# Kernel optimization log

Measured on AMD Instinct MI355X. Metric: run time of the kernel, lower is better.

## Reference

```python
import jax, jax.numpy as jnp
import numpy as np

B, T, D, R = 4, 2048, 512, 1024
N_INNER, N_B = 9, 2          # inner pool bins, boundary pool bins (roipool_size='2_9')
RATIO = 1.0 / 5.0            # boundary extension ratio passed to BRoI1DPool
NB = N_B + N_INNER + N_B     # 13 total bins: [start bins | inner bins | end bins]


def _bin_centers(a, b, n):
    # a, b: (B, R) -> (B, R, n) centers of n equal bins covering [a, b]
    i = (jnp.arange(n, dtype=a.dtype) + 0.5) / n
    return a[..., None] + i * (b - a)[..., None]


def broi1d_pool(feats, rois):
    # Boundary ROI 1D pooling: feats (B, T, D), rois (B, R, 2) -> (B, R, D, NB).
    # Each bin samples its center position via linear interpolation along T.
    s, e = rois[..., 0], rois[..., 1]
    ext = RATIO * (e - s)
    pos = jnp.concatenate([
        _bin_centers(s - ext, s + ext, N_B),
        _bin_centers(s, e, N_INNER),
        _bin_centers(e - ext, e + ext, N_B)], axis=-1)          # (B, R, NB)
    pos = jnp.clip(pos, 0.0, T - 1)
    lo = jnp.floor(pos).astype(jnp.int32)
    hi = jnp.minimum(lo + 1, T - 1)
    w = (pos - lo.astype(pos.dtype))[..., None]

    def gather(idx):
        g = jnp.take_along_axis(feats, idx.reshape(idx.shape[0], -1)[..., None], axis=1)
        return g.reshape(idx.shape + (feats.shape[-1],))          # (B, R, NB, D)

    vals = (1.0 - w) * gather(lo) + w * gather(hi)
    return vals.transpose(0, 1, 3, 2)                              # (B, R, D, NB)


def setup_inputs():
    key = jax.random.key(0)
    ks = jax.random.split(key, 10)
    features = jax.random.normal(ks[0], (B, T, D), jnp.float32)

    def make_rois(k):
        k1, k2 = jax.random.split(k)
        s = jax.random.uniform(k1, (B, R), jnp.float32, 0.0, T - 300.0)
        L = 16.0 + jax.random.uniform(k2, (B, R), jnp.float32) * 256.0
        return jnp.stack([s, s + L], axis=-1)

    rois = make_rois(ks[1])
    start_rois = make_rois(ks[2])
    end_rois = make_rois(ks[3])
    rois_mask = jnp.ones((B, R), jnp.float32)
    rois_pos_emb = jax.random.normal(ks[4], (B, R, D), jnp.float32)

    d_left = (N_B + N_INNER // 2 + 1) * D
    W_left = jax.random.normal(ks[5], (D, d_left), jnp.float32) / np.sqrt(d_left).astype(np.float32)
    b_left = jnp.zeros((D,), jnp.float32)
    W_inner = jax.random.normal(ks[6], (D, N_INNER * D), jnp.float32) / np.sqrt(N_INNER * D).astype(np.float32)
    b_inner = jnp.zeros((D,), jnp.float32)
    W_roi = jax.random.normal(ks[7], (D, 2 * D), jnp.float32) / np.sqrt(2 * D).astype(np.float32)
    b_roi = jnp.zeros((D,), jnp.float32)
    return {"features": features, "start_rois": start_rois, "end_rois": end_rois,
            "rois": rois, "rois_mask": rois_mask, "rois_pos_emb": rois_pos_emb,
            "W_left": W_left, "b_left": b_left, "W_inner": W_inner, "b_inner": b_inner,
            "W_roi": W_roi, "b_roi": b_roi}


def reference(features, start_rois, end_rois, rois, rois_mask, rois_pos_emb,
              W_left, b_left, W_inner, b_inner, W_roi, b_roi):
    pooled = broi1d_pool(features, rois)          # (B, R, D, NB)
    mb, r = pooled.shape[:2]

    def fc(x, W, b):
        # Linear + Dropout(eval=identity) + SELU
        return jax.nn.selu(x @ W.T + b)

    left = fc(pooled[:, :, :, 0:N_INNER // 2 + N_B + 1].reshape(mb, r, -1), W_left, b_left)
    inner = fc(pooled[:, :, :, N_B:N_INNER + N_B].reshape(mb, r, -1), W_inner, b_inner)
    # NOTE: the original code reuses left_fc for the right branch (right_fc is dead).
    right = fc(pooled[:, :, :, N_INNER // 2 + N_B:N_INNER + 2 * N_B].reshape(mb, r, -1), W_left, b_left)
    return fc(jnp.concatenate([right - left, inner], axis=2), W_roi, b_roi)  # (B, R, D)
```

## Files before the change

kernel.cpp:

```cpp
#include <hip/hip_runtime.h>
#include <hip/hip_bf16.h>
#include <cstdint>
#include <cmath>

#define BB 4
#define TT 2048
#define DD 512
#define RR 1024
#define MM (BB*RR)
#define NBINS 13
#define LDXP (NBINS*DD)

typedef __bf16 bf16;
typedef bf16 bf16x8 __attribute__((ext_vector_type(8)));
typedef bf16 bf16x2 __attribute__((ext_vector_type(2)));
typedef float f32x4 __attribute__((ext_vector_type(4)));

__device__ __forceinline__ float selu_f(float x) {
    const float sc = 1.0507009873554805f;
    const float aa = 1.6732632423543772f;
    return x > 0.0f ? sc * x : sc * aa * (expf(x) - 1.0f);
}

__device__ __forceinline__ void gload_lds16(const bf16* g, bf16* l) {
    __builtin_amdgcn_global_load_lds(
        (const __attribute__((address_space(1))) void*)g,
        (__attribute__((address_space(3))) void*)l, 16, 0, 0);
}

template<int N>
__device__ __forceinline__ void wait_vm() {
    if constexpr (N == 0)      asm volatile("s_waitcnt vmcnt(0)" ::: "memory");
    else if constexpr (N == 4) asm volatile("s_waitcnt vmcnt(4)" ::: "memory");
    else if constexpr (N == 6) asm volatile("s_waitcnt vmcnt(6)" ::: "memory");
}

template<int ROWS>
__device__ __forceinline__ void stage_tile64(const bf16* __restrict__ src, int lda,
                                             bf16* tile, int tid) {
#pragma unroll
    for (int it = 0; it < ROWS / 32; ++it) {
        int idx = it * 256 + tid;
        int row = idx >> 3;
        int col = ((idx & 7) ^ (row & 7)) * 8;
        bf16* wavebase = tile + (idx & ~63) * 8;
        gload_lds16(src + (size_t)row * lda + col, wavebase);
    }
}

__device__ __forceinline__ bf16x8 frd64(const bf16* tile, int row, int s) {
    int p = s ^ (row & 7);
    return *(const bf16x8*)(tile + row * 64 + p * 8);
}

template<int NB_, int KT>
__device__ __forceinline__ void w_row_body(const float* __restrict__ Wsrc,
                                           bf16* __restrict__ Wdst,
                                           float* ld, int n, int tid) {
    const float* src = Wsrc + (size_t)n * KT;
    for (int i = tid; i < KT; i += 256) ld[i] = src[i];
    __syncthreads();
    bf16* dst = Wdst + (size_t)n * KT;
    for (int i = tid; i < KT; i += 256) {
        int bin = i >> 9, d = i & 511;
        dst[i] = (bf16)ld[d * NB_ + bin];
    }
}

__device__ __forceinline__ void pool_body(const float* __restrict__ feats,
                                          const float* __restrict__ rois,
                                          bf16* __restrict__ Xp, int m, int tid) {
    int b = m >> 10;
    float s = rois[2 * m];
    float e = rois[2 * m + 1];
    float ext = 0.2f * (e - s);
    int d0 = tid * 2;
    bf16* orow = Xp + (size_t)m * LDXP + d0;
    const float* fb = feats + (size_t)b * TT * DD + d0;
#pragma unroll
    for (int j = 0; j < NBINS; ++j) {
        float pos;
        if (j < 2)       pos = (s - ext) + ((float)j + 0.5f) * ext;
        else if (j < 11) pos = s + (((float)(j - 2) + 0.5f) * (1.0f / 9.0f)) * (e - s);
        else             pos = (e - ext) + ((float)(j - 11) + 0.5f) * ext;
        pos = fminf(fmaxf(pos, 0.0f), (float)(TT - 1));
        float fl = floorf(pos);
        int lo = (int)fl;
        int hi = lo + 1; if (hi > TT - 1) hi = TT - 1;
        float w = pos - fl;
        float2 vlo = *(const float2*)(fb + (size_t)lo * DD);
        float2 vhi = *(const float2*)(fb + (size_t)hi * DD);
        bf16x2 o;
        o.x = (bf16)((1.0f - w) * vlo.x + w * vhi.x);
        o.y = (bf16)((1.0f - w) * vlo.y + w * vhi.y);
        *(bf16x2*)(orow + j * DD) = o;
    }
}

__global__ __launch_bounds__(256) void prep_all(
    const float* __restrict__ feats, const float* __restrict__ rois,
    const float* __restrict__ W_left, const float* __restrict__ W_inner,
    const float* __restrict__ W_roi,
    bf16* __restrict__ Xp, bf16* __restrict__ Wl, bf16* __restrict__ Wi,
    bf16* __restrict__ Wr)
{
    __shared__ float ld[4608];
    int bid = blockIdx.x, tid = threadIdx.x;
    if (bid < 4096) {
        pool_body(feats, rois, Xp, bid, tid);
    } else if (bid < 4608) {
        w_row_body<7, 3584>(W_left, Wl, ld, bid - 4096, tid);
    } else if (bid < 5120) {
        w_row_body<9, 4608>(W_inner, Wi, ld, bid - 4608, tid);
    } else {
        int i0 = (bid - 5120) * 1024 + tid * 4;
        float4 v = *(const float4*)(W_roi + i0);
        bf16* d = Wr + i0;
        d[0] = (bf16)v.x; d[1] = (bf16)v.y; d[2] = (bf16)v.z; d[3] = (bf16)v.w;
    }
}


template<int K, bool OUT_BF16>
__device__ __forceinline__ void gemm_single_body(
    const bf16* __restrict__ A, int lda,
    const bf16* __restrict__ Bw, const float* __restrict__ bias,
    void* __restrict__ Out, int ldo, int ocol0,
    bf16* sm, int m0, int n0)
{
    int tid = threadIdx.x, lane = tid & 63, w = tid >> 6;
    int wr = w >> 1, wc = w & 1;
    const bf16* Ab = A + (size_t)m0 * lda;
    const bf16* Bb = Bw + (size_t)n0 * K;
    int frow = lane & 15, sl = lane >> 4;
    f32x4 acc[2][2] = {};
    bf16 *A0 = sm,        *B0 = sm + 4096;
    bf16 *A1 = sm + 8192, *B1 = sm + 12288;

    auto stage = [&](bf16* ap, bf16* bp, int t) {
        stage_tile64<64>(Ab + t * 64, lda, ap, tid);
        stage_tile64<64>(Bb + t * 64, K, bp, tid);
    };
    auto step = [&](bf16* ap, bf16* bp, int t, bool dostage) {
        __builtin_amdgcn_s_barrier();
        bf16x8 af[2][2], bfr[2][2];
#pragma unroll
        for (int ks = 0; ks < 2; ++ks) {
#pragma unroll
            for (int mf = 0; mf < 2; ++mf) af[ks][mf] = frd64(ap, wr * 32 + mf * 16 + frow, ks * 4 + sl);
#pragma unroll
            for (int nf = 0; nf < 2; ++nf) bfr[ks][nf] = frd64(bp, wc * 32 + nf * 16 + frow, ks * 4 + sl);
        }
        asm volatile("s_waitcnt lgkmcnt(0)" ::: "memory");
        __builtin_amdgcn_sched_barrier(0);
        __builtin_amdgcn_s_barrier();
        if (dostage) stage(ap, bp, t + 2);
        __builtin_amdgcn_s_setprio(1);
#pragma unroll
        for (int ks = 0; ks < 2; ++ks)
#pragma unroll
            for (int mf = 0; mf < 2; ++mf)
#pragma unroll
                for (int nf = 0; nf < 2; ++nf)
                    acc[mf][nf] = __builtin_amdgcn_mfma_f32_16x16x32_bf16(af[ks][mf], bfr[ks][nf], acc[mf][nf], 0, 0, 0);
        __builtin_amdgcn_s_setprio(0);
    };

    constexpr int NT = K / 64;
    stage(A0, B0, 0);
    stage(A1, B1, 1);
    for (int t = 0; t + 2 < NT; t += 2) {
        wait_vm<4>(); step(A0, B0, t, true);
        wait_vm<4>(); step(A1, B1, t + 1, true);
    }
    wait_vm<4>(); step(A0, B0, NT - 2, false);
    wait_vm<0>(); step(A1, B1, NT - 1, false);

    int crow = (lane >> 4) * 4;
    int ccol = lane & 15;
#pragma unroll
    for (int mf = 0; mf < 2; ++mf) {
#pragma unroll
        for (int nf = 0; nf < 2; ++nf) {
            int col = n0 + wc * 32 + nf * 16 + ccol;
            float bv = bias[col];
#pragma unroll
            for (int r2 = 0; r2 < 4; ++r2) {
                int row = m0 + wr * 32 + mf * 16 + crow + r2;
                float v = selu_f(acc[mf][nf][r2] + bv);
                if constexpr (OUT_BF16)
                    ((bf16*)Out)[(size_t)row * ldo + ocol0 + col] = (bf16)v;
                else
                    ((float*)Out)[(size_t)row * ldo + ocol0 + col] = v;
            }
        }
    }
}

template<int K>
__device__ __forceinline__ void gemm_dual_body(
    const bf16* __restrict__ Xp, const bf16* __restrict__ Wl,
    const float* __restrict__ bias, bf16* __restrict__ Y,
    bf16* sm, int m0, int n0)
{
    int tid = threadIdx.x, lane = tid & 63, w = tid >> 6;
    int wr = w >> 1, wc = w & 1;
    const bf16* AL = Xp + (size_t)m0 * LDXP;
    const bf16* AR = AL + 3072;
    const bf16* Bb = Wl + (size_t)n0 * K;
    int frow = lane & 15, sl = lane >> 4;
    f32x4 accL[2][2] = {}, accR[2][2] = {};
    bf16 *L0 = sm,         *R0 = sm + 4096,  *B0 = sm + 8192;
    bf16 *L1 = sm + 12288, *R1 = sm + 16384, *B1 = sm + 20480;

    auto stage = [&](bf16* lp, bf16* rp, bf16* bp, int t) {
        stage_tile64<64>(AL + t * 64, LDXP, lp, tid);
        stage_tile64<64>(AR + t * 64, LDXP, rp, tid);
        stage_tile64<64>(Bb + t * 64, K, bp, tid);
    };
    auto step = [&](bf16* lp, bf16* rp, bf16* bp, int t, bool dostage) {
        __builtin_amdgcn_s_barrier();
        bf16x8 afL[2][2], afR[2][2], bfr[2][2];
#pragma unroll
        for (int ks = 0; ks < 2; ++ks) {
#pragma unroll
            for (int mf = 0; mf < 2; ++mf) {
                afL[ks][mf] = frd64(lp, wr * 32 + mf * 16 + frow, ks * 4 + sl);
                afR[ks][mf] = frd64(rp, wr * 32 + mf * 16 + frow, ks * 4 + sl);
            }
#pragma unroll
            for (int nf = 0; nf < 2; ++nf) bfr[ks][nf] = frd64(bp, wc * 32 + nf * 16 + frow, ks * 4 + sl);
        }
        asm volatile("s_waitcnt lgkmcnt(0)" ::: "memory");
        __builtin_amdgcn_sched_barrier(0);
        __builtin_amdgcn_s_barrier();
        if (dostage) stage(lp, rp, bp, t + 2);
        __builtin_amdgcn_s_setprio(1);
#pragma unroll
        for (int ks = 0; ks < 2; ++ks)
#pragma unroll
            for (int mf = 0; mf < 2; ++mf)
#pragma unroll
                for (int nf = 0; nf < 2; ++nf) {
                    accL[mf][nf] = __builtin_amdgcn_mfma_f32_16x16x32_bf16(afL[ks][mf], bfr[ks][nf], accL[mf][nf], 0, 0, 0);
                    accR[mf][nf] = __builtin_amdgcn_mfma_f32_16x16x32_bf16(afR[ks][mf], bfr[ks][nf], accR[mf][nf], 0, 0, 0);
                }
        __builtin_amdgcn_s_setprio(0);
    };

    constexpr int NT = K / 64;
    stage(L0, R0, B0, 0);
    stage(L1, R1, B1, 1);
    for (int t = 0; t + 2 < NT; t += 2) {
        wait_vm<6>(); step(L0, R0, B0, t, true);
        wait_vm<6>(); step(L1, R1, B1, t + 1, true);
    }
    wait_vm<6>(); step(L0, R0, B0, NT - 2, false);
    wait_vm<0>(); step(L1, R1, B1, NT - 1, false);

    int crow = (lane >> 4) * 4;
    int ccol = lane & 15;
#pragma unroll
    for (int mf = 0; mf < 2; ++mf) {
#pragma unroll
        for (int nf = 0; nf < 2; ++nf) {
            int col = n0 + wc * 32 + nf * 16 + ccol;
            float bv = bias[col];
#pragma unroll
            for (int r2 = 0; r2 < 4; ++r2) {
                int row = m0 + wr * 32 + mf * 16 + crow + r2;
                float vL = selu_f(accL[mf][nf][r2] + bv);
                float vR = selu_f(accR[mf][nf][r2] + bv);
                Y[(size_t)row * 1024 + col] = (bf16)(vR - vL);
            }
        }
    }
}

__global__ __launch_bounds__(256) void wide_gemm(
    const bf16* __restrict__ Xp, const bf16* __restrict__ Wl,
    const float* __restrict__ bl, const bf16* __restrict__ Wi,
    const float* __restrict__ bi, bf16* __restrict__ Y)
{
    __shared__ bf16 sm[24576];
    int bid = blockIdx.x;
    if (bid < 512) {
        gemm_dual_body<3584>(Xp, Wl, bl, Y, sm, (bid & 63) * 64, (bid >> 6) * 64);
    } else {
        int b2 = bid - 512;
        gemm_single_body<4608, true>(Xp + 1024, LDXP, Wi, bi, (void*)Y, 1024, 512,
                                     sm, (b2 & 63) * 64, (b2 >> 6) * 64);
    }
}

__global__ __launch_bounds__(256) void final_gemm(
    const bf16* __restrict__ Y, const bf16* __restrict__ Wr,
    const float* __restrict__ br, float* __restrict__ out)
{
    __shared__ bf16 sm[16384];
    int bid = blockIdx.x;
    gemm_single_body<1024, false>(Y, 1024, Wr, br, (void*)out, 512, 0,
                                  sm, (bid & 63) * 64, (bid >> 6) * 64);
}

extern "C" void kernel_launch(void* const* d_in, const int* in_sizes, int n_in,
                              void* d_out, int out_size, void* d_ws, size_t ws_size,
                              hipStream_t stream) {
    const float* feats   = (const float*)d_in[0];
    const float* rois    = (const float*)d_in[3];
    const float* W_left  = (const float*)d_in[6];
    const float* b_left  = (const float*)d_in[7];
    const float* W_inner = (const float*)d_in[8];
    const float* b_inner = (const float*)d_in[9];
    const float* W_roi   = (const float*)d_in[10];
    const float* b_roi   = (const float*)d_in[11];
    float* out = (float*)d_out;

    bf16* wsb = (bf16*)d_ws;
    constexpr size_t XP_ELEMS = (size_t)MM * LDXP;
    constexpr size_t WL_ELEMS = (size_t)512 * 3584;
    constexpr size_t WI_ELEMS = (size_t)512 * 4608;
    constexpr size_t WR_ELEMS = (size_t)512 * 1024;
    bf16* Xp = wsb;
    bf16* Wl = Xp + XP_ELEMS;
    bf16* Wi = Wl + WL_ELEMS;
    bf16* Wr = Wi + WI_ELEMS;
    bf16* Y  = Wr + WR_ELEMS;

    prep_all<<<5632, 256, 0, stream>>>(feats, rois, W_left, W_inner, W_roi,
                                       Xp, Wl, Wi, Wr);
    wide_gemm<<<1024, 256, 0, stream>>>(Xp, Wl, b_left, Wi, b_inner, Y);
    final_gemm<<<512, 256, 0, stream>>>(Y, Wr, b_roi, out);
}
```

Before: 113.3 us.

## Enlarge GEMM tiles to 128x64 and pipeline K in 32-wide half-tile stages

The GEMM tiles grow from 64x64 to 128x64 rows per block, and each 64-wide K step is split into two 32-wide halves with their own swizzle. Loads of the next half are interleaved with MFMA work on the current half under finer vmcnt waits and barriers. This is meant to raise operand reuse per LDS load and hide global latency better. In exchange it halves the grid (512 and 256 blocks on a 256-CU part), raises LDS and accumulator register use, and adds more barriers per K step.

```diff
diff --git a/kernel.cpp b/kernel.cpp
--- a/kernel.cpp
+++ b/kernel.cpp
@@ -30,27 +30,34 @@
 
 template<int N>
 __device__ __forceinline__ void wait_vm() {
-    if constexpr (N == 0)      asm volatile("s_waitcnt vmcnt(0)" ::: "memory");
-    else if constexpr (N == 4) asm volatile("s_waitcnt vmcnt(4)" ::: "memory");
-    else if constexpr (N == 6) asm volatile("s_waitcnt vmcnt(6)" ::: "memory");
+    if constexpr (N == 0)       asm volatile("s_waitcnt vmcnt(0)" ::: "memory");
+    else if constexpr (N == 3)  asm volatile("s_waitcnt vmcnt(3)" ::: "memory");
+    else if constexpr (N == 5)  asm volatile("s_waitcnt vmcnt(5)" ::: "memory");
+    else if constexpr (N == 6)  asm volatile("s_waitcnt vmcnt(6)" ::: "memory");
+    else if constexpr (N == 10) asm volatile("s_waitcnt vmcnt(10)" ::: "memory");
+}
+
+__device__ __forceinline__ void lgkm_fence() {
+    asm volatile("s_waitcnt lgkmcnt(0)" ::: "memory");
+    __builtin_amdgcn_sched_barrier(0);
 }
 
 template<int ROWS>
-__device__ __forceinline__ void stage_tile64(const bf16* __restrict__ src, int lda,
-                                             bf16* tile, int tid) {
-#pragma unroll
-    for (int it = 0; it < ROWS / 32; ++it) {
+__device__ __forceinline__ void stage_half(const bf16* __restrict__ src, int lda,
+                                           bf16* dst, int tid) {
+#pragma unroll
+    for (int it = 0; it < ROWS / 64; ++it) {
         int idx = it * 256 + tid;
-        int row = idx >> 3;
-        int col = ((idx & 7) ^ (row & 7)) * 8;
-        bf16* wavebase = tile + (idx & ~63) * 8;
+        int row = idx >> 2;
+        int col = ((idx & 3) ^ ((row >> 1) & 3)) * 8;
+        bf16* wavebase = dst + (idx & ~63) * 8;
         gload_lds16(src + (size_t)row * lda + col, wavebase);
     }
 }
 
-__device__ __forceinline__ bf16x8 frd64(const bf16* tile, int row, int s) {
-    int p = s ^ (row & 7);
-    return *(const bf16x8*)(tile + row * 64 + p * 8);
+__device__ __forceinline__ bf16x8 frd32(const bf16* half, int row, int sl) {
+    int p = sl ^ ((row >> 1) & 3);
+    return *(const bf16x8*)(half + row * 32 + p * 8);
 }
 
 template<int NB_, int KT>
@@ -133,60 +140,74 @@
     const bf16* Ab = A + (size_t)m0 * lda;
     const bf16* Bb = Bw + (size_t)n0 * K;
     int frow = lane & 15, sl = lane >> 4;
-    f32x4 acc[2][2] = {};
-    bf16 *A0 = sm,        *B0 = sm + 4096;
-    bf16 *A1 = sm + 8192, *B1 = sm + 12288;
-
-    auto stage = [&](bf16* ap, bf16* bp, int t) {
-        stage_tile64<64>(Ab + t * 64, lda, ap, tid);
-        stage_tile64<64>(Bb + t * 64, K, bp, tid);
-    };
-    auto step = [&](bf16* ap, bf16* bp, int t, bool dostage) {
-        __builtin_amdgcn_s_barrier();
-        bf16x8 af[2][2], bfr[2][2];
-#pragma unroll
-        for (int ks = 0; ks < 2; ++ks) {
-#pragma unroll
-            for (int mf = 0; mf < 2; ++mf) af[ks][mf] = frd64(ap, wr * 32 + mf * 16 + frow, ks * 4 + sl);
-#pragma unroll
-            for (int nf = 0; nf < 2; ++nf) bfr[ks][nf] = frd64(bp, wc * 32 + nf * 16 + frow, ks * 4 + sl);
-        }
-        asm volatile("s_waitcnt lgkmcnt(0)" ::: "memory");
-        __builtin_amdgcn_sched_barrier(0);
-        __builtin_amdgcn_s_barrier();
-        if (dostage) stage(ap, bp, t + 2);
+    f32x4 acc[4][2] = {};
+    bf16 *buf0 = sm, *buf1 = sm + 12288;
+
+    auto stageH = [&](bf16* p, int u, int h) {
+        stage_half<128>(Ab + u * 64 + h * 32, lda, p + h * 4096, tid);
+        stage_half<64>(Bb + u * 64 + h * 32, K, p + 8192 + h * 2048, tid);
+    };
+    auto rdA = [&](bf16* p, int h, bf16x8 (&af)[4]) {
+#pragma unroll
+        for (int mf = 0; mf < 4; ++mf)
+            af[mf] = frd32(p + h * 4096, wr * 64 + mf * 16 + frow, sl);
+    };
+    auto rdB = [&](bf16* p, int h, bf16x8 (&bfr)[2]) {
+#pragma unroll
+        for (int nf = 0; nf < 2; ++nf)
+            bfr[nf] = frd32(p + 8192 + h * 2048, wc * 32 + nf * 16 + frow, sl);
+    };
+    auto mm = [&](bf16x8 (&af)[4], bf16x8 (&bfr)[2]) {
         __builtin_amdgcn_s_setprio(1);
 #pragma unroll
-        for (int ks = 0; ks < 2; ++ks)
-#pragma unroll
-            for (int mf = 0; mf < 2; ++mf)
-#pragma unroll
-                for (int nf = 0; nf < 2; ++nf)
-                    acc[mf][nf] = __builtin_amdgcn_mfma_f32_16x16x32_bf16(af[ks][mf], bfr[ks][nf], acc[mf][nf], 0, 0, 0);
+        for (int mf = 0; mf < 4; ++mf)
+#pragma unroll
+            for (int nf = 0; nf < 2; ++nf)
+                acc[mf][nf] = __builtin_amdgcn_mfma_f32_16x16x32_bf16(af[mf], bfr[nf], acc[mf][nf], 0, 0, 0);
         __builtin_amdgcn_s_setprio(0);
     };
 
+    auto tileS = [&](bf16* b, bf16* nb, int t, int mode) {
+        bf16x8 af[4], bfr[2];
+        if (mode <= 1) stageH(nb, t + 1, 1);
+        rdA(b, 0, af); rdB(b, 0, bfr);
+        if (mode <= 1) wait_vm<6>(); else wait_vm<0>();
+        __builtin_amdgcn_s_barrier();
+        lgkm_fence();
+        mm(af, bfr);
+        __builtin_amdgcn_s_barrier();
+        if (mode == 0) stageH(b, t + 2, 0);
+        rdA(b, 1, af); rdB(b, 1, bfr);
+        if (mode == 0) wait_vm<6>(); else if (mode == 1) wait_vm<3>();
+        __builtin_amdgcn_s_barrier();
+        lgkm_fence();
+        mm(af, bfr);
+        __builtin_amdgcn_s_barrier();
+    };
+
     constexpr int NT = K / 64;
-    stage(A0, B0, 0);
-    stage(A1, B1, 1);
-    for (int t = 0; t + 2 < NT; t += 2) {
-        wait_vm<4>(); step(A0, B0, t, true);
-        wait_vm<4>(); step(A1, B1, t + 1, true);
-    }
-    wait_vm<4>(); step(A0, B0, NT - 2, false);
-    wait_vm<0>(); step(A1, B1, NT - 1, false);
+    stageH(buf0, 0, 0); stageH(buf0, 0, 1); stageH(buf1, 1, 0);
+    wait_vm<6>();
+    __builtin_amdgcn_s_barrier();
+    int t = 0;
+    for (; t + 2 < NT; ++t) {
+        bf16 *b = (t & 1) ? buf1 : buf0, *nb = (t & 1) ? buf0 : buf1;
+        tileS(b, nb, t, 0);
+    }
+    { bf16 *b = (t & 1) ? buf1 : buf0, *nb = (t & 1) ? buf0 : buf1; tileS(b, nb, t, 1); ++t; }
+    { bf16 *b = (t & 1) ? buf1 : buf0, *nb = (t & 1) ? buf0 : buf1; tileS(b, nb, t, 2); }
 
     int crow = (lane >> 4) * 4;
     int ccol = lane & 15;
 #pragma unroll
-    for (int mf = 0; mf < 2; ++mf) {
+    for (int mf = 0; mf < 4; ++mf) {
 #pragma unroll
         for (int nf = 0; nf < 2; ++nf) {
             int col = n0 + wc * 32 + nf * 16 + ccol;
             float bv = bias[col];
 #pragma unroll
             for (int r2 = 0; r2 < 4; ++r2) {
-                int row = m0 + wr * 32 + mf * 16 + crow + r2;
+                int row = m0 + wr * 64 + mf * 16 + crow + r2;
                 float v = selu_f(acc[mf][nf][r2] + bv);
                 if constexpr (OUT_BF16)
                     ((bf16*)Out)[(size_t)row * ldo + ocol0 + col] = (bf16)v;
@@ -209,66 +230,90 @@
     const bf16* AR = AL + 3072;
     const bf16* Bb = Wl + (size_t)n0 * K;
     int frow = lane & 15, sl = lane >> 4;
-    f32x4 accL[2][2] = {}, accR[2][2] = {};
-    bf16 *L0 = sm,         *R0 = sm + 4096,  *B0 = sm + 8192;
-    bf16 *L1 = sm + 12288, *R1 = sm + 16384, *B1 = sm + 20480;
-
-    auto stage = [&](bf16* lp, bf16* rp, bf16* bp, int t) {
-        stage_tile64<64>(AL + t * 64, LDXP, lp, tid);
-        stage_tile64<64>(AR + t * 64, LDXP, rp, tid);
-        stage_tile64<64>(Bb + t * 64, K, bp, tid);
-    };
-    auto step = [&](bf16* lp, bf16* rp, bf16* bp, int t, bool dostage) {
-        __builtin_amdgcn_s_barrier();
-        bf16x8 afL[2][2], afR[2][2], bfr[2][2];
-#pragma unroll
-        for (int ks = 0; ks < 2; ++ks) {
-#pragma unroll
-            for (int mf = 0; mf < 2; ++mf) {
-                afL[ks][mf] = frd64(lp, wr * 32 + mf * 16 + frow, ks * 4 + sl);
-                afR[ks][mf] = frd64(rp, wr * 32 + mf * 16 + frow, ks * 4 + sl);
-            }
-#pragma unroll
-            for (int nf = 0; nf < 2; ++nf) bfr[ks][nf] = frd64(bp, wc * 32 + nf * 16 + frow, ks * 4 + sl);
-        }
-        asm volatile("s_waitcnt lgkmcnt(0)" ::: "memory");
-        __builtin_amdgcn_sched_barrier(0);
-        __builtin_amdgcn_s_barrier();
-        if (dostage) stage(lp, rp, bp, t + 2);
+    f32x4 accL[4][2] = {}, accR[4][2] = {};
+    bf16 *buf0 = sm, *buf1 = sm + 20480;
+
+    auto stageH = [&](bf16* p, int u, int h) {
+        stage_half<128>(AL + u * 64 + h * 32, LDXP, p + h * 4096, tid);
+        stage_half<128>(AR + u * 64 + h * 32, LDXP, p + 8192 + h * 4096, tid);
+        stage_half<64>(Bb + u * 64 + h * 32, K, p + 16384 + h * 2048, tid);
+    };
+    auto rdL = [&](bf16* p, int h, bf16x8 (&af)[4]) {
+#pragma unroll
+        for (int mf = 0; mf < 4; ++mf)
+            af[mf] = frd32(p + h * 4096, wr * 64 + mf * 16 + frow, sl);
+    };
+    auto rdR = [&](bf16* p, int h, bf16x8 (&af)[4]) {
+#pragma unroll
+        for (int mf = 0; mf < 4; ++mf)
+            af[mf] = frd32(p + 8192 + h * 4096, wr * 64 + mf * 16 + frow, sl);
+    };
+    auto rdB = [&](bf16* p, int h, bf16x8 (&bfr)[2]) {
+#pragma unroll
+        for (int nf = 0; nf < 2; ++nf)
+            bfr[nf] = frd32(p + 16384 + h * 2048, wc * 32 + nf * 16 + frow, sl);
+    };
+    auto mm = [&](bf16x8 (&af)[4], bf16x8 (&bfr)[2], f32x4 (&ac)[4][2]) {
         __builtin_amdgcn_s_setprio(1);
 #pragma unroll
-        for (int ks = 0; ks < 2; ++ks)
-#pragma unroll
-            for (int mf = 0; mf < 2; ++mf)
-#pragma unroll
-                for (int nf = 0; nf < 2; ++nf) {
-                    accL[mf][nf] = __builtin_amdgcn_mfma_f32_16x16x32_bf16(afL[ks][mf], bfr[ks][nf], accL[mf][nf], 0, 0, 0);
-                    accR[mf][nf] = __builtin_amdgcn_mfma_f32_16x16x32_bf16(afR[ks][mf], bfr[ks][nf], accR[mf][nf], 0, 0, 0);
-                }
+        for (int mf = 0; mf < 4; ++mf)
+#pragma unroll
+            for (int nf = 0; nf < 2; ++nf)
+                ac[mf][nf] = __builtin_amdgcn_mfma_f32_16x16x32_bf16(af[mf], bfr[nf], ac[mf][nf], 0, 0, 0);
         __builtin_amdgcn_s_setprio(0);
     };
 
+    auto tileD = [&](bf16* b, bf16* nb, int t, int mode) {
+        bf16x8 af[4], bfr[2];
+        if (mode <= 1) stageH(nb, t + 1, 1);
+        rdL(b, 0, af); rdB(b, 0, bfr);
+        __builtin_amdgcn_s_barrier();
+        lgkm_fence();
+        mm(af, bfr, accL);
+        __builtin_amdgcn_s_barrier();
+        rdR(b, 0, af);
+        if (mode <= 1) wait_vm<10>(); else wait_vm<0>();
+        __builtin_amdgcn_s_barrier();
+        lgkm_fence();
+        mm(af, bfr, accR);
+        __builtin_amdgcn_s_barrier();
+        if (mode == 0) stageH(b, t + 2, 0);
+        rdL(b, 1, af); rdB(b, 1, bfr);
+        __builtin_amdgcn_s_barrier();
+        lgkm_fence();
+        mm(af, bfr, accL);
+        __builtin_amdgcn_s_barrier();
+        rdR(b, 1, af);
+        if (mode == 0) wait_vm<10>(); else if (mode == 1) wait_vm<5>();
+        __builtin_amdgcn_s_barrier();
+        lgkm_fence();
+        mm(af, bfr, accR);
+        __builtin_amdgcn_s_barrier();
+    };
+
     constexpr int NT = K / 64;
-    stage(L0, R0, B0, 0);
-    stage(L1, R1, B1, 1);
-    for (int t = 0; t + 2 < NT; t += 2) {
-        wait_vm<6>(); step(L0, R0, B0, t, true);
-        wait_vm<6>(); step(L1, R1, B1, t + 1, true);
-    }
-    wait_vm<6>(); step(L0, R0, B0, NT - 2, false);
-    wait_vm<0>(); step(L1, R1, B1, NT - 1, false);
+    stageH(buf0, 0, 0); stageH(buf0, 0, 1); stageH(buf1, 1, 0);
+    wait_vm<10>();
+    __builtin_amdgcn_s_barrier();
+    int t = 0;
+    for (; t + 2 < NT; ++t) {
+        bf16 *b = (t & 1) ? buf1 : buf0, *nb = (t & 1) ? buf0 : buf1;
+        tileD(b, nb, t, 0);
+    }
+    { bf16 *b = (t & 1) ? buf1 : buf0, *nb = (t & 1) ? buf0 : buf1; tileD(b, nb, t, 1); ++t; }
+    { bf16 *b = (t & 1) ? buf1 : buf0, *nb = (t & 1) ? buf0 : buf1; tileD(b, nb, t, 2); }
 
     int crow = (lane >> 4) * 4;
     int ccol = lane & 15;
 #pragma unroll
-    for (int mf = 0; mf < 2; ++mf) {
+    for (int mf = 0; mf < 4; ++mf) {
 #pragma unroll
         for (int nf = 0; nf < 2; ++nf) {
             int col = n0 + wc * 32 + nf * 16 + ccol;
             float bv = bias[col];
 #pragma unroll
             for (int r2 = 0; r2 < 4; ++r2) {
-                int row = m0 + wr * 32 + mf * 16 + crow + r2;
+                int row = m0 + wr * 64 + mf * 16 + crow + r2;
                 float vL = selu_f(accL[mf][nf][r2] + bv);
                 float vR = selu_f(accR[mf][nf][r2] + bv);
                 Y[(size_t)row * 1024 + col] = (bf16)(vR - vL);
@@ -282,14 +327,14 @@
     const float* __restrict__ bl, const bf16* __restrict__ Wi,
     const float* __restrict__ bi, bf16* __restrict__ Y)
 {
-    __shared__ bf16 sm[24576];
+    __shared__ bf16 sm[40960];
     int bid = blockIdx.x;
-    if (bid < 512) {
-        gemm_dual_body<3584>(Xp, Wl, bl, Y, sm, (bid & 63) * 64, (bid >> 6) * 64);
+    if (bid < 256) {
+        gemm_dual_body<3584>(Xp, Wl, bl, Y, sm, (bid & 31) * 128, (bid >> 5) * 64);
     } else {
-        int b2 = bid - 512;
+        int b2 = bid - 256;
         gemm_single_body<4608, true>(Xp + 1024, LDXP, Wi, bi, (void*)Y, 1024, 512,
-                                     sm, (b2 & 63) * 64, (b2 >> 6) * 64);
+                                     sm, (b2 & 31) * 128, (b2 >> 5) * 64);
     }
 }
 
@@ -297,10 +342,10 @@
     const bf16* __restrict__ Y, const bf16* __restrict__ Wr,
     const float* __restrict__ br, float* __restrict__ out)
 {
-    __shared__ bf16 sm[16384];
+    __shared__ bf16 sm[24576];
     int bid = blockIdx.x;
     gemm_single_body<1024, false>(Y, 1024, Wr, br, (void*)out, 512, 0,
-                                  sm, (bid & 63) * 64, (bid >> 6) * 64);
+                                  sm, (bid & 31) * 128, (bid >> 5) * 64);
 }
 
 extern "C" void kernel_launch(void* const* d_in, const int* in_sizes, int n_in,
@@ -329,6 +374,6 @@
 
     prep_all<<<5632, 256, 0, stream>>>(feats, rois, W_left, W_inner, W_roi,
                                        Xp, Wl, Wi, Wr);
-    wide_gemm<<<1024, 256, 0, stream>>>(Xp, Wl, b_left, Wi, b_inner, Y);
-    final_gemm<<<512, 256, 0, stream>>>(Y, Wr, b_roi, out);
-}
+    wide_gemm<<<512, 256, 0, stream>>>(Xp, Wl, b_left, Wi, b_inner, Y);
+    final_gemm<<<256, 256, 0, stream>>>(Y, Wr, b_roi, out);
+}
```

Result: slower. 128.1 us (+13.1%).
